# Kernel optimization log

Measured on AMD Instinct MI355X. Metric: run time of the kernel, lower is better.

The kernel has to match this reference:

```python
import jax, jax.numpy as jnp
import numpy as np

MARGIN = 0.2
EPS = 1e-6  # torch.pairwise_distance adds eps to the difference before the norm


def setup_inputs() -> dict:
    key = jax.random.key(0)
    k1, k2, k3 = jax.random.split(key, 3)
    B, D = 8192, 128
    emb1 = jax.random.normal(k1, (B, D), dtype=jnp.float32)
    emb2 = jax.random.normal(k2, (B, D), dtype=jnp.float32)
    target = jax.random.randint(k3, (B,), 0, 2, dtype=jnp.int64)
    return {"emb1": emb1, "emb2": emb2, "target": target}


def reference(emb1, emb2, target):
    B, D = emb1.shape
    # torch.pairwise_distance(a, b) = ||a - b + EPS||_2; expand the square:
    # |a-b+eps|^2 = |a|^2 + |b|^2 - 2 a.b + 2*eps*(sum(a)-sum(b)) + D*eps^2
    sq = (
        jnp.sum(emb1 * emb1, axis=-1)[:, None]
        + jnp.sum(emb2 * emb2, axis=-1)[None, :]
        - 2.0 * (emb1 @ emb2.T)
        + 2.0 * EPS * (jnp.sum(emb1, axis=-1)[:, None] - jnp.sum(emb2, axis=-1)[None, :])
        + D * EPS * EPS
    )
    dist = jnp.sqrt(jnp.maximum(sq, 0.0))  # [B, B]: dist[i, j] = ||emb1[i] - emb2[j] + eps||

    pos = target == 1
    neg = target == 0
    # hardest positive: max over columns j with target[j]==1; hardest negative: min over target[j]==0
    pos_max = jnp.max(jnp.where(pos[None, :], dist, -jnp.inf), axis=1)  # [B]
    neg_min = jnp.min(jnp.where(neg[None, :], dist, jnp.inf), axis=1)   # [B]
    per_anchor = jnp.maximum(pos_max - neg_min + MARGIN, 0.0)
    anchor_w = pos.astype(dist.dtype)
    # mean over anchors (rows i with target[i]==1)
    return jnp.sum(per_anchor * anchor_w) / jnp.sum(anchor_w)
```

## Files before the change

### kernel.cpp

```cpp
#include <hip/hip_runtime.h>
#include <hip/hip_bf16.h>
#include <math.h>


#define DDIM   128
#define SPLITS 8
#define MARGIN 0.2f
#define EPS    1e-6f
#define SENT   1e30f

#define CHUNK_PITCH 1056
#define WAVE_SPAN   (8 * CHUNK_PITCH)
#define TILE_BYTES  (4 * WAVE_SPAN)

typedef unsigned short ushort_t;
typedef __attribute__((ext_vector_type(8))) short short8;
typedef __attribute__((ext_vector_type(4))) float f32x4;
typedef __attribute__((ext_vector_type(4))) unsigned short ushort4_t;

__device__ __forceinline__ ushort_t f2bf(float f) {
    unsigned int u = __float_as_uint(f);
    u = (u + 0x7FFFu + ((u >> 16) & 1u)) >> 16;
    return (ushort_t)u;
}

__device__ __forceinline__ void g2lds16(const ushort_t* g, void* lds) {
    __builtin_amdgcn_global_load_lds(
        (const __attribute__((address_space(1))) unsigned int*)g,
        (__attribute__((address_space(3))) unsigned int*)lds,
        16, 0, 0);
}

__global__ void prep_kernel(const float* __restrict__ e1, const float* __restrict__ e2,
                            const int* __restrict__ target,
                            ushort_t* __restrict__ e1b, ushort_t* __restrict__ e2b,
                            float* __restrict__ rowterm,
                            float* __restrict__ cpos, float* __restrict__ cneg,
                            float* __restrict__ redsum, int* __restrict__ ticket,
                            int* __restrict__ rbTicket, int B) {
    if (blockIdx.x == 0) {
        int t = threadIdx.x;
        if (t < B / 128) rbTicket[t] = 0;
        else if (t == 64) { redsum[0] = 0.f; redsum[1] = 0.f; }
        else if (t == 65) *ticket = 0;
    }
    int gr  = blockIdx.x * 32 + (threadIdx.x >> 3);
    int seg = threadIdx.x & 7;
    bool first = gr < B;
    int r = first ? gr : gr - B;
    const float* src = (first ? e1 : e2) + (size_t)r * DDIM;
    ushort_t*    dst = (first ? e1b : e2b) + (size_t)r * DDIM;
    const float sc = first ? -2.f : 1.f;
    float s = 0.f, n = 0.f;
    #pragma unroll
    for (int it = 0; it < 4; ++it) {
        int e0 = (seg + it * 8) * 4;
        float4 v = *(const float4*)(src + e0);
        ushort4_t o;
        o.x = f2bf(sc * v.x); o.y = f2bf(sc * v.y);
        o.z = f2bf(sc * v.z); o.w = f2bf(sc * v.w);
        *(ushort4_t*)(dst + e0) = o;
        s += v.x + v.y + v.z + v.w;
        n += v.x * v.x + v.y * v.y + v.z * v.z + v.w * v.w;
    }
    #pragma unroll
    for (int m = 1; m <= 4; m <<= 1) {
        s += __shfl_xor(s, m, 64);
        n += __shfl_xor(n, m, 64);
    }
    if (seg == 0) {
        if (first) {
            rowterm[r] = n + 2.f * EPS * s + (float)DDIM * EPS * EPS;
        } else {
            float ct = n - 2.f * EPS * s;
            int tg = target[r];
            cpos[r] = (tg == 1) ? ct : -SENT;
            cneg[r] = (tg == 0) ? ct :  SENT;
        }
    }
}

__device__ __forceinline__ void stage_tile_dma(const ushort_t* __restrict__ gRow0,
                                               unsigned char* __restrict__ lds,
                                               int w, int l) {
    const ushort_t* g = gRow0 + (size_t)(w * 32) * DDIM + l * 8;
    unsigned char* lp = lds + w * WAVE_SPAN;
    #pragma unroll
    for (int it = 0; it < 8; ++it)
        g2lds16(g + it * 512, lp + it * CHUNK_PITCH);
}

__global__ __launch_bounds__(256, 2)
void tile_kernel(const ushort_t* __restrict__ e1b, const ushort_t* __restrict__ e2b,
                 const float* __restrict__ cpos, const float* __restrict__ cneg,
                 const float* __restrict__ rowterm, const int* __restrict__ target,
                 float* __restrict__ pmp, float* __restrict__ nmp,
                 int* __restrict__ rbTicket, float* __restrict__ redsum,
                 int* __restrict__ ticket, float* __restrict__ out, int B) {
    __shared__ __align__(16) unsigned char Bs[2][TILE_BYTES];

    const int tid = threadIdx.x;
    const int w   = tid >> 6;
    const int l   = tid & 63;
    const int lq  = l >> 4;
    const int lm  = l & 15;
    const int row0 = blockIdx.x * 128;
    const int colSpan = B / SPLITS;
    const int col0 = blockIdx.y * colSpan;
    const int nTiles = colSpan / 128;

    const int wr = (w >> 1) * 64;
    const int wc = (w & 1) * 64;

    const unsigned char* bLane0 = Bs[0] + ((wc >> 2) + (lm >> 2)) * CHUNK_PITCH
                                        + (lm & 3) * 256 + lq * 16;

    const ushort_t* aG = e1b + (size_t)(row0 + wr + lm) * DDIM + lq * 8;
    short8 afr[4][4];
    #pragma unroll
    for (int i = 0; i < 4; ++i)
        #pragma unroll
        for (int k4 = 0; k4 < 4; ++k4)
            afr[i][k4] = *(const short8*)(aG + i * 16 * DDIM + k4 * 32);

    stage_tile_dma(e2b + (size_t)col0 * DDIM, Bs[0], w, l);

    float pm[4][4], nm[4][4];
    #pragma unroll
    for (int i = 0; i < 4; ++i)
        #pragma unroll
        for (int r = 0; r < 4; ++r) { pm[i][r] = -SENT; nm[i][r] = SENT; }

    __syncthreads();

    for (int t = 0; t < nTiles; ++t) {
        if (t + 1 < nTiles)
            stage_tile_dma(e2b + (size_t)(col0 + (t + 1) * 128) * DDIM,
                           Bs[(t + 1) & 1], w, l);

        const unsigned char* bl = bLane0 + (t & 1) * TILE_BYTES;

        f32x4 acc[4][4];
        #pragma unroll
        for (int i = 0; i < 4; ++i)
            #pragma unroll
            for (int j = 0; j < 4; ++j)
                acc[i][j] = (f32x4){0.f, 0.f, 0.f, 0.f};

        #pragma unroll
        for (int kk = 0; kk < DDIM; kk += 32) {
            const int k4 = kk >> 5;
            const int ko = kk * 2;
            short8 bf[4];
            #pragma unroll
            for (int j = 0; j < 4; ++j)
                bf[j] = *(const short8*)(bl + j * (4 * CHUNK_PITCH) + ko);
            #pragma unroll
            for (int i = 0; i < 4; ++i)
                #pragma unroll
                for (int j = 0; j < 4; ++j)
                    acc[i][j] = __builtin_amdgcn_mfma_f32_16x16x32_bf16(
                                    afr[i][k4], bf[j], acc[i][j], 0, 0, 0);
        }

        {
            const int colb = col0 + t * 128 + wc + lm;
            #pragma unroll
            for (int jp = 0; jp < 2; ++jp) {
                const int j0 = 2 * jp, j1 = j0 + 1;
                const float cp0 = cpos[colb + j0 * 16], cn0 = cneg[colb + j0 * 16];
                const float cp1 = cpos[colb + j1 * 16], cn1 = cneg[colb + j1 * 16];
                #pragma unroll
                for (int i = 0; i < 4; ++i)
                    #pragma unroll
                    for (int r = 0; r < 4; ++r) {
                        const float d0 = acc[i][j0][r];
                        const float d1 = acc[i][j1][r];
                        pm[i][r] = fmaxf(fmaxf(pm[i][r], d0 + cp0), d1 + cp1);
                        nm[i][r] = fminf(fminf(nm[i][r], d0 + cn0), d1 + cn1);
                    }
            }
        }

        __syncthreads();
    }

    #pragma unroll
    for (int m = 1; m < 16; m <<= 1) {
        #pragma unroll
        for (int i = 0; i < 4; ++i)
            #pragma unroll
            for (int r = 0; r < 4; ++r) {
                pm[i][r] = fmaxf(pm[i][r], __shfl_xor(pm[i][r], m, 64));
                nm[i][r] = fminf(nm[i][r], __shfl_xor(nm[i][r], m, 64));
            }
    }

    float* smP = (float*)Bs;
    float* smN = smP + 128;
    if ((w & 1) == 1 && lm == 0) {
        #pragma unroll
        for (int i = 0; i < 4; ++i)
            #pragma unroll
            for (int r = 0; r < 4; ++r) {
                int lr = wr + i * 16 + lq * 4 + r;
                smP[lr] = pm[i][r];
                smN[lr] = nm[i][r];
            }
    }
    __syncthreads();
    if ((w & 1) == 0 && lm == 0) {
        #pragma unroll
        for (int i = 0; i < 4; ++i)
            #pragma unroll
            for (int r = 0; r < 4; ++r) {
                int lr  = wr + i * 16 + lq * 4 + r;
                int row = row0 + lr;
                pmp[(size_t)blockIdx.y * B + row] = fmaxf(pm[i][r], smP[lr]);
                nmp[(size_t)blockIdx.y * B + row] = fminf(nm[i][r], smN[lr]);
            }
    }

    __shared__ int lastrb;
    __syncthreads();
    if (tid == 0) {
        __threadfence();
        int prev = __hip_atomic_fetch_add(&rbTicket[blockIdx.x], 1,
                       __ATOMIC_ACQ_REL, __HIP_MEMORY_SCOPE_AGENT);
        lastrb = (prev == SPLITS - 1);
    }
    __syncthreads();
    if (!lastrb) return;

    float s = 0.f, c = 0.f;
    if (tid < 128) {
        int row = row0 + tid;
        float pmv = -SENT, nmv = SENT;
        #pragma unroll
        for (int sp = 0; sp < SPLITS; ++sp) {
            pmv = fmaxf(pmv, __hip_atomic_load(&pmp[(size_t)sp * B + row],
                              __ATOMIC_RELAXED, __HIP_MEMORY_SCOPE_AGENT));
            nmv = fminf(nmv, __hip_atomic_load(&nmp[(size_t)sp * B + row],
                              __ATOMIC_RELAXED, __HIP_MEMORY_SCOPE_AGENT));
        }
        float rt = rowterm[row];
        float dp = sqrtf(fmaxf(rt + pmv, 0.f));
        float dn = sqrtf(fmaxf(rt + nmv, 0.f));
        if (target[row] == 1) {
            s = fmaxf(dp - dn + MARGIN, 0.f);
            c = 1.f;
        }
    }
    #pragma unroll
    for (int off = 32; off > 0; off >>= 1) {
        s += __shfl_down(s, off, 64);
        c += __shfl_down(c, off, 64);
    }
    __shared__ float ls[4], lc[4];
    if (l == 0) { ls[w] = s; lc[w] = c; }
    __syncthreads();
    if (tid == 0) {
        float ss = ls[0] + ls[1] + ls[2] + ls[3];
        float cc = lc[0] + lc[1] + lc[2] + lc[3];
        atomicAdd(&redsum[0], ss);
        atomicAdd(&redsum[1], cc);
        __threadfence();
        int done = atomicAdd(ticket, 1);
        if (done == (B / 128) - 1) {
            __threadfence();
            float fs = __hip_atomic_load(&redsum[0], __ATOMIC_RELAXED, __HIP_MEMORY_SCOPE_AGENT);
            float fc = __hip_atomic_load(&redsum[1], __ATOMIC_RELAXED, __HIP_MEMORY_SCOPE_AGENT);
            out[0] = fs / fc;
        }
    }
}

extern "C" void kernel_launch(void* const* d_in, const int* in_sizes, int n_in,
                              void* d_out, int out_size, void* d_ws, size_t ws_size,
                              hipStream_t stream) {
    const float* e1     = (const float*)d_in[0];
    const float* e2     = (const float*)d_in[1];
    const int*   target = (const int*)d_in[2];
    float* out = (float*)d_out;
    const int B = in_sizes[2];

    char* p = (char*)d_ws;
    ushort_t* e1b  = (ushort_t*)p;   p += (size_t)B * DDIM * 2;
    ushort_t* e2b  = (ushort_t*)p;   p += (size_t)B * DDIM * 2;
    float* rowterm = (float*)p;      p += (size_t)B * 4;
    float* cpos    = (float*)p;      p += (size_t)B * 4;
    float* cneg    = (float*)p;      p += (size_t)B * 4;
    float* pmp     = (float*)p;      p += (size_t)SPLITS * B * 4;
    float* nmp     = (float*)p;      p += (size_t)SPLITS * B * 4;
    float* redsum  = (float*)p;      p += 2 * 4;
    int*   ticket  = (int*)p;        p += 4;
    int*   rbTicket= (int*)p;        p += (size_t)(B / 128) * 4;

    {
        int blocks = (2 * B) / 32;
        prep_kernel<<<blocks, 256, 0, stream>>>(e1, e2, target, e1b, e2b,
                                                rowterm, cpos, cneg,
                                                redsum, ticket, rbTicket, B);
    }
    {
        dim3 grid(B / 128, SPLITS);
        tile_kernel<<<grid, 256, 0, stream>>>(e1b, e2b, cpos, cneg,
                                              rowterm, target, pmp, nmp,
                                              rbTicket, redsum, ticket, out, B);
    }
}
```

Baseline: 104.2 us.

## Drop LDS staging and load B fragments directly from global memory

Removes the double-buffered LDS tile and the global_load_lds DMA, so each wave now reads its bf16 B fragments straight from global memory (relying on L2/L1 caching) and the per-tile barriers go away. The column tile shrinks to 64 with a 64x32 per-wave output, SPLITS doubles to 16 to add more blocks, and launch bounds allow 3 blocks per CU. This trades LDS traffic and syncs for more global/cache loads with less reuse per wave, and the loads are no longer prefetched ahead of the MFMAs.

After: 147.4 us. 41.5% more time.

```diff
diff --git a/kernel.cpp b/kernel.cpp
--- a/kernel.cpp
+++ b/kernel.cpp
@@ -4,14 +4,10 @@
 
 
 #define DDIM   128
-#define SPLITS 8
+#define SPLITS 16
 #define MARGIN 0.2f
 #define EPS    1e-6f
 #define SENT   1e30f
-
-#define CHUNK_PITCH 1056
-#define WAVE_SPAN   (8 * CHUNK_PITCH)
-#define TILE_BYTES  (4 * WAVE_SPAN)
 
 typedef unsigned short ushort_t;
 typedef __attribute__((ext_vector_type(8))) short short8;
@@ -22,13 +18,6 @@
     unsigned int u = __float_as_uint(f);
     u = (u + 0x7FFFu + ((u >> 16) & 1u)) >> 16;
     return (ushort_t)u;
-}
-
-__device__ __forceinline__ void g2lds16(const ushort_t* g, void* lds) {
-    __builtin_amdgcn_global_load_lds(
-        (const __attribute__((address_space(1))) unsigned int*)g,
-        (__attribute__((address_space(3))) unsigned int*)lds,
-        16, 0, 0);
 }
 
 __global__ void prep_kernel(const float* __restrict__ e1, const float* __restrict__ e2,
@@ -80,25 +69,13 @@
     }
 }
 
-__device__ __forceinline__ void stage_tile_dma(const ushort_t* __restrict__ gRow0,
-                                               unsigned char* __restrict__ lds,
-                                               int w, int l) {
-    const ushort_t* g = gRow0 + (size_t)(w * 32) * DDIM + l * 8;
-    unsigned char* lp = lds + w * WAVE_SPAN;
-    #pragma unroll
-    for (int it = 0; it < 8; ++it)
-        g2lds16(g + it * 512, lp + it * CHUNK_PITCH);
-}
-
-__global__ __launch_bounds__(256, 2)
+__global__ __launch_bounds__(256, 3)
 void tile_kernel(const ushort_t* __restrict__ e1b, const ushort_t* __restrict__ e2b,
                  const float* __restrict__ cpos, const float* __restrict__ cneg,
                  const float* __restrict__ rowterm, const int* __restrict__ target,
                  float* __restrict__ pmp, float* __restrict__ nmp,
                  int* __restrict__ rbTicket, float* __restrict__ redsum,
                  int* __restrict__ ticket, float* __restrict__ out, int B) {
-    __shared__ __align__(16) unsigned char Bs[2][TILE_BYTES];
-
     const int tid = threadIdx.x;
     const int w   = tid >> 6;
     const int l   = tid & 63;
@@ -107,13 +84,10 @@
     const int row0 = blockIdx.x * 128;
     const int colSpan = B / SPLITS;
     const int col0 = blockIdx.y * colSpan;
-    const int nTiles = colSpan / 128;
+    const int nTiles = colSpan / 64;
 
     const int wr = (w >> 1) * 64;
-    const int wc = (w & 1) * 64;
-
-    const unsigned char* bLane0 = Bs[0] + ((wc >> 2) + (lm >> 2)) * CHUNK_PITCH
-                                        + (lm & 3) * 256 + lq * 16;
+    const int wc = (w & 1) * 32;
 
     const ushort_t* aG = e1b + (size_t)(row0 + wr + lm) * DDIM + lq * 8;
     short8 afr[4][4];
@@ -123,7 +97,7 @@
         for (int k4 = 0; k4 < 4; ++k4)
             afr[i][k4] = *(const short8*)(aG + i * 16 * DDIM + k4 * 32);
 
-    stage_tile_dma(e2b + (size_t)col0 * DDIM, Bs[0], w, l);
+    const ushort_t* bG = e2b + (size_t)(col0 + wc + lm) * DDIM + lq * 8;
 
     float pm[4][4], nm[4][4];
     #pragma unroll
@@ -131,58 +105,44 @@
         #pragma unroll
         for (int r = 0; r < 4; ++r) { pm[i][r] = -SENT; nm[i][r] = SENT; }
 
-    __syncthreads();
-
     for (int t = 0; t < nTiles; ++t) {
-        if (t + 1 < nTiles)
-            stage_tile_dma(e2b + (size_t)(col0 + (t + 1) * 128) * DDIM,
-                           Bs[(t + 1) & 1], w, l);
-
-        const unsigned char* bl = bLane0 + (t & 1) * TILE_BYTES;
-
-        f32x4 acc[4][4];
-        #pragma unroll
-        for (int i = 0; i < 4; ++i)
-            #pragma unroll
-            for (int j = 0; j < 4; ++j)
+        const ushort_t* bT = bG + (size_t)t * 64 * DDIM;
+
+        f32x4 acc[4][2];
+        #pragma unroll
+        for (int i = 0; i < 4; ++i)
+            #pragma unroll
+            for (int j = 0; j < 2; ++j)
                 acc[i][j] = (f32x4){0.f, 0.f, 0.f, 0.f};
 
         #pragma unroll
-        for (int kk = 0; kk < DDIM; kk += 32) {
-            const int k4 = kk >> 5;
-            const int ko = kk * 2;
-            short8 bf[4];
-            #pragma unroll
-            for (int j = 0; j < 4; ++j)
-                bf[j] = *(const short8*)(bl + j * (4 * CHUNK_PITCH) + ko);
+        for (int k4 = 0; k4 < 4; ++k4) {
+            short8 bf[2];
+            #pragma unroll
+            for (int j = 0; j < 2; ++j)
+                bf[j] = *(const short8*)(bT + j * 16 * DDIM + k4 * 32);
             #pragma unroll
             for (int i = 0; i < 4; ++i)
                 #pragma unroll
-                for (int j = 0; j < 4; ++j)
+                for (int j = 0; j < 2; ++j)
                     acc[i][j] = __builtin_amdgcn_mfma_f32_16x16x32_bf16(
                                     afr[i][k4], bf[j], acc[i][j], 0, 0, 0);
         }
 
         {
-            const int colb = col0 + t * 128 + wc + lm;
-            #pragma unroll
-            for (int jp = 0; jp < 2; ++jp) {
-                const int j0 = 2 * jp, j1 = j0 + 1;
-                const float cp0 = cpos[colb + j0 * 16], cn0 = cneg[colb + j0 * 16];
-                const float cp1 = cpos[colb + j1 * 16], cn1 = cneg[colb + j1 * 16];
+            const int colb = col0 + t * 64 + wc + lm;
+            const float cp0 = cpos[colb],      cn0 = cneg[colb];
+            const float cp1 = cpos[colb + 16], cn1 = cneg[colb + 16];
+            #pragma unroll
+            for (int i = 0; i < 4; ++i)
                 #pragma unroll
-                for (int i = 0; i < 4; ++i)
-                    #pragma unroll
-                    for (int r = 0; r < 4; ++r) {
-                        const float d0 = acc[i][j0][r];
-                        const float d1 = acc[i][j1][r];
-                        pm[i][r] = fmaxf(fmaxf(pm[i][r], d0 + cp0), d1 + cp1);
-                        nm[i][r] = fminf(fminf(nm[i][r], d0 + cn0), d1 + cn1);
-                    }
-            }
-        }
-
-        __syncthreads();
+                for (int r = 0; r < 4; ++r) {
+                    const float d0 = acc[i][0][r];
+                    const float d1 = acc[i][1][r];
+                    pm[i][r] = fmaxf(fmaxf(pm[i][r], d0 + cp0), d1 + cp1);
+                    nm[i][r] = fminf(fminf(nm[i][r], d0 + cn0), d1 + cn1);
+                }
+        }
     }
 
     #pragma unroll
@@ -196,8 +156,7 @@
             }
     }
 
-    float* smP = (float*)Bs;
-    float* smN = smP + 128;
+    __shared__ float smP[128], smN[128];
     if ((w & 1) == 1 && lm == 0) {
         #pragma unroll
         for (int i = 0; i < 4; ++i)
```
